# Performance work log

Measured on AMD Instinct MI355X. Metric: run time of the kernel, lower is better.

## Reference

```python
import jax, jax.numpy as jnp
import numpy as np
from jax import lax

EDGES = [(11,12),(11,23),(12,24),(23,24),(23,25),(25,27),(24,26),(26,28),(11,13),(13,15),(12,14),(14,16)]
J = 33

def _build_neighbors():
    nb = [[j] for j in range(J)]
    for a, b in EDGES:
        nb[a].append(b); nb[b].append(a)
    K = max(len(n) for n in nb)
    idx = np.zeros((J, K), np.int32)
    msk = np.zeros((J, K), np.float32)
    for j, n in enumerate(nb):
        idx[j, :len(n)] = n; msk[j, :len(n)] = 1.0
    return jnp.asarray(idx), jnp.asarray(msk)

NBR_IDX, NBR_MASK = _build_neighbors()
BN_EPS = 1e-5

def conv(x, w, b):
    y = lax.conv_general_dilated(x, w, (1, 1), 'SAME', dimension_numbers=('NCHW', 'OIHW', 'NCHW'))
    return y + b[None, :, None, None]

def bn(x, g, b):
    # eval-mode BatchNorm with running_mean=0, running_var=1
    s = g / jnp.sqrt(1.0 + BN_EPS)
    return x * s[None, :, None, None] + b[None, :, None, None]

def maxpool2(x):
    return lax.reduce_window(x, -jnp.inf, lax.max, (1, 1, 2, 2), (1, 1, 2, 2), 'VALID')

def deconv2x2(x, w, b):
    # ConvTranspose2d(k=2, s=2): w is [Cin, Cout, 2, 2]
    y = jnp.einsum('bcij,codk->boidjk', x, w)
    B, O, H, _, W, _ = y.shape
    return y.reshape(B, O, 2 * H, 2 * W) + b[None, :, None, None]

def forward(x, conv1_w, conv1_b, bn1_g, bn1_b, conv2_w, conv2_b, bn2_g, bn2_b,
            conv3_w, conv3_b, bn3_g, bn3_b, conv4_w, conv4_b, bn4_g, bn4_b,
            dc1_w, dc1_b, dc2_w, dc2_b, head_w, head_b, proj_w, proj_b,
            msg_w, msg_b, gru_w_ih, gru_w_hh, gru_b_ih, gru_b_hh,
            refine_w, refine_b, vis_w1, vis_b1, vis_w2, vis_b2):
    relu = jax.nn.relu
    h = bn(relu(conv(x, conv1_w, conv1_b)), bn1_g, bn1_b)
    h = bn(relu(conv(h, conv2_w, conv2_b)), bn2_g, bn2_b)
    h = maxpool2(h)
    h = bn(relu(conv(h, conv3_w, conv3_b)), bn3_g, bn3_b)
    h = maxpool2(h)
    enc = bn(relu(conv(h, conv4_w, conv4_b)), bn4_g, bn4_b)  # [B,256,H/4,W/4]
    f = relu(deconv2x2(enc, dc1_w, dc1_b))
    feat_map = relu(deconv2x2(f, dc2_w, dc2_b))  # [B,64,H,W]
    init_hm = jax.nn.sigmoid(conv(feat_map, head_w, head_b))  # [B,J,H,W]
    B, Jn, H, W = init_hm.shape
    sm = jax.nn.softmax(init_hm.reshape(B, Jn, H * W) / 0.1, axis=-1).reshape(B, Jn, H, W)
    w_idx = jnp.linspace(0.0, 1.0, W)
    h_idx = jnp.linspace(0.0, 1.0, H)
    pred_x = (sm.sum(-2) * w_idx).sum(-1)  # [B,J] in [0,1]
    pred_y = (sm.sum(-1) * h_idx).sum(-1)
    # grid_sample bilinear, align_corners=True: grid=(2p-1) -> pixel coord p*(dim-1)
    ix = pred_x * (W - 1)
    iy = pred_y * (H - 1)
    x0 = jnp.clip(jnp.floor(ix), 0, W - 1)
    y0 = jnp.clip(jnp.floor(iy), 0, H - 1)
    wx = ix - x0
    wy = iy - y0
    x0i = x0.astype(jnp.int32); x1i = jnp.clip(x0i + 1, 0, W - 1)
    y0i = y0.astype(jnp.int32); y1i = jnp.clip(y0i + 1, 0, H - 1)
    fm = feat_map.transpose(0, 2, 3, 1)  # [B,H,W,C]
    bidx = jnp.arange(B)[:, None]
    v00 = fm[bidx, y0i, x0i]; v01 = fm[bidx, y0i, x1i]
    v10 = fm[bidx, y1i, x0i]; v11 = fm[bidx, y1i, x1i]
    wx = wx[..., None]; wy = wy[..., None]
    joint = (v00 * (1 - wx) * (1 - wy) + v01 * wx * (1 - wy)
             + v10 * (1 - wx) * wy + v11 * wx * wy)  # [B,J,64]
    joint_feats = joint @ proj_w.T + proj_b
    # SkeletonGNN (all joints read original joint_feats -> fully parallel)
    gathered = joint_feats[:, NBR_IDX, :]  # [B,J,K,D]
    lin = gathered @ msg_w.T + msg_b
    m = NBR_MASK[None, :, :, None]
    msgs = (lin * m).sum(2) / NBR_MASK.sum(1)[None, :, None]  # [B,J,D]
    gi = msgs @ gru_w_ih.T + gru_b_ih
    gh = joint_feats @ gru_w_hh.T + gru_b_hh
    D = joint_feats.shape[-1]
    ir, iz, inn = gi[..., :D], gi[..., D:2 * D], gi[..., 2 * D:]
    hr, hz, hn = gh[..., :D], gh[..., D:2 * D], gh[..., 2 * D:]
    r = jax.nn.sigmoid(ir + hr)
    z = jax.nn.sigmoid(iz + hz)
    n = jnp.tanh(inn + r * hn)
    refined_feats = (1 - z) * n + z * joint_feats
    refined_bias = refined_feats.mean(-1)[:, :, None, None]
    refined_hm = jax.nn.sigmoid(conv(init_hm, refine_w, refine_b) + refined_bias)
    # visibility head: adaptive avg pool to 4x4 (enc HW divisible by 4), eval dropout = identity
    eB, eC, eH, eW = enc.shape
    p = enc.reshape(eB, eC, 4, eH // 4, 4, eW // 4).mean((3, 5))  # [B,256,4,4]
    v = jax.nn.relu(p.reshape(eB, -1) @ vis_w1.T + vis_b1)
    vis_pred = jax.nn.sigmoid(v @ vis_w2.T + vis_b2)
    return refined_hm, vis_pred

def setup_inputs() -> dict:
    key = jax.random.key(0)
    ks = iter(jax.random.split(key, 64))
    def w(shape, s=0.05):
        return (jax.random.normal(next(ks), shape, dtype=jnp.float32) * s)
    inp = {
        'x': jax.random.normal(next(ks), (16, 3, 256, 256), dtype=jnp.float32),
        'conv1_w': w((32, 3, 3, 3)), 'conv1_b': w((32,)), 'bn1_g': jnp.ones((32,)), 'bn1_b': jnp.zeros((32,)),
        'conv2_w': w((64, 32, 3, 3)), 'conv2_b': w((64,)), 'bn2_g': jnp.ones((64,)), 'bn2_b': jnp.zeros((64,)),
        'conv3_w': w((128, 64, 3, 3)), 'conv3_b': w((128,)), 'bn3_g': jnp.ones((128,)), 'bn3_b': jnp.zeros((128,)),
        'conv4_w': w((256, 128, 3, 3)), 'conv4_b': w((256,)), 'bn4_g': jnp.ones((256,)), 'bn4_b': jnp.zeros((256,)),
        'dc1_w': w((256, 128, 2, 2)), 'dc1_b': w((128,)),
        'dc2_w': w((128, 64, 2, 2)), 'dc2_b': w((64,)),
        'head_w': w((33, 64, 1, 1)), 'head_b': w((33,)),
        'proj_w': w((64, 64)), 'proj_b': w((64,)),
        'msg_w': w((64, 64)), 'msg_b': w((64,)),
        'gru_w_ih': w((192, 64)), 'gru_w_hh': w((192, 64)),
        'gru_b_ih': w((192,)), 'gru_b_hh': w((192,)),
        'refine_w': w((33, 33, 3, 3)), 'refine_b': w((33,)),
        'vis_w1': w((256, 256 * 16)), 'vis_b1': w((256,)),
        'vis_w2': w((33, 256)), 'vis_b2': w((33,)),
    }
    return inp

def reference(x, conv1_w, conv1_b, bn1_g, bn1_b, conv2_w, conv2_b, bn2_g, bn2_b,
              conv3_w, conv3_b, bn3_g, bn3_b, conv4_w, conv4_b, bn4_g, bn4_b,
              dc1_w, dc1_b, dc2_w, dc2_b, head_w, head_b, proj_w, proj_b,
              msg_w, msg_b, gru_w_ih, gru_w_hh, gru_b_ih, gru_b_hh,
              refine_w, refine_b, vis_w1, vis_b1, vis_w2, vis_b2):
    return forward(x, conv1_w, conv1_b, bn1_g, bn1_b, conv2_w, conv2_b, bn2_g, bn2_b,
                   conv3_w, conv3_b, bn3_g, bn3_b, conv4_w, conv4_b, bn4_g, bn4_b,
                   dc1_w, dc1_b, dc2_w, dc2_b, head_w, head_b, proj_w, proj_b,
                   msg_w, msg_b, gru_w_ih, gru_w_hh, gru_b_ih, gru_b_hh,
                   refine_w, refine_b, vis_w1, vis_b1, vis_w2, vis_b2)
```

## Files before the change

kernel.cpp:

```cpp
#include <hip/hip_runtime.h>
#include <hip/hip_bf16.h>
#include <math.h>

#define BN_RS 0.99999500003749977f

typedef __attribute__((ext_vector_type(8))) __bf16 bf16x8;
typedef __attribute__((ext_vector_type(4))) float f32x4;

union U16 { uint4 u; bf16x8 v; __hip_bfloat16 h[8]; };

__device__ __forceinline__ float sigf(float v) { return 1.0f / (1.0f + expf(-v)); }

__global__ __launch_bounds__(256)
void repack_conv_w_k(const float* __restrict__ w, __hip_bfloat16* __restrict__ wb,
                     int taps, int Co, int Ci, int CoT, int Kp)
{
    int i = blockIdx.x * 256 + threadIdx.x;
    int tot = taps * CoT * Kp;
    if (i >= tot) return;
    int k = i % Kp, n = (i / Kp) % CoT, t = i / (Kp * CoT);
    float v = (n < Co && k < Ci) ? w[((long)n * Ci + k) * taps + t] : 0.0f;
    wb[i] = __float2bfloat16(v);
}
__global__ __launch_bounds__(256)
void repack_deconv_w_k(const float* __restrict__ w, __hip_bfloat16* __restrict__ wb,
                       int Co, int Ci)
{
    int i = blockIdx.x * 256 + threadIdx.x;
    int tot = 4 * Co * Ci;
    if (i >= tot) return;
    int k = i % Ci, n = (i / Ci) % Co, q = i / (Ci * Co);
    wb[i] = __float2bfloat16(w[((long)k * Co + n) * 4 + q]);
}

__global__ __launch_bounds__(256)
void conv1_k(const float* __restrict__ x, const float* __restrict__ w,
             const float* __restrict__ cb, const float* __restrict__ g,
             const float* __restrict__ bb, __hip_bfloat16* __restrict__ out)
{
    __shared__ float sw[216];
    const int tid = threadIdx.x;
    const int b = blockIdx.z >> 2, cg = blockIdx.z & 3, co0 = cg * 8;
    for (int i = tid; i < 216; i += 256) {
        int t = i % 9, co = (i / 9) % 8, ci = i / 72;
        sw[i] = w[((co0 + co) * 3 + ci) * 9 + t];
    }
    __syncthreads();
    const int tx = tid & 15, ty = tid >> 4;
    const int y = blockIdx.y * 16 + ty;
    const int xs = blockIdx.x * 64 + tx;
    float acc[4][8];
#pragma unroll
    for (int p = 0; p < 4; ++p)
#pragma unroll
        for (int c = 0; c < 8; ++c) acc[p][c] = 0.0f;
    for (int ci = 0; ci < 3; ++ci) {
        const float* plane = x + ((long)b * 3 + ci) * 65536;
#pragma unroll
        for (int t = 0; t < 9; ++t) {
            const int dy = t / 3 - 1, dx = t % 3 - 1;
            const int yy = y + dy;
            if ((unsigned)yy < 256u) {
                const float* row = plane + yy * 256;
                float ws[8];
#pragma unroll
                for (int c = 0; c < 8; ++c) ws[c] = sw[ci * 72 + c * 9 + t];
#pragma unroll
                for (int p = 0; p < 4; ++p) {
                    const int xx = xs + p * 16 + dx;
                    const float v = ((unsigned)xx < 256u) ? row[xx] : 0.0f;
#pragma unroll
                    for (int c = 0; c < 8; ++c) acc[p][c] = fmaf(v, ws[c], acc[p][c]);
                }
            }
        }
    }
#pragma unroll
    for (int p = 0; p < 4; ++p) {
        U16 o;
#pragma unroll
        for (int c = 0; c < 8; ++c) {
            const int cc = co0 + c;
            float v = fmaxf(acc[p][c] + cb[cc], 0.0f) * (g[cc] * BN_RS) + bb[cc];
            o.h[c] = __float2bfloat16(v);
        }
        *(uint4*)(void*)(out + (((long)b * 65536 + (long)y * 256 + xs + p * 16) * 32 + co0)) = o.u;
    }
}

template<int MODE>
__global__ __launch_bounds__(256)
void mfma_conv_k(const __hip_bfloat16* __restrict__ in,
                 const __hip_bfloat16* __restrict__ wb,
                 const float* __restrict__ cbias,
                 const float* __restrict__ bng, const float* __restrict__ bnb,
                 const float* __restrict__ ebias,
                 __hip_bfloat16* __restrict__ out_bf, float* __restrict__ out_f32,
                 int H, int W, int Cin, int CoutT, int CG, int S)
{
    extern __shared__ float ltr[];
    const int tid = threadIdx.x;
    const int wid = tid >> 6, lane = tid & 63;
    const int ln = lane & 15, kg = lane >> 4;
    const int u = blockIdx.x * 4 + wid;
    const int y = u / S, x0 = (u % S) * 64;
    const int b = blockIdx.z / CG, cg = blockIdx.z % CG;
    const int co0 = cg * 64;
    const int KC = Cin >> 5;
    const long inb = (long)b * H * W * Cin;

    f32x4 acc[4][4];
#pragma unroll
    for (int i = 0; i < 4; ++i)
#pragma unroll
        for (int j = 0; j < 4; ++j) acc[i][j] = f32x4{0.f, 0.f, 0.f, 0.f};

    constexpr int NT = (MODE == 1) ? 1 : 9;
    for (int kc = 0; kc < KC; ++kc) {
        const int kofs = kc * 32 + kg * 8;
#pragma unroll
        for (int t = 0; t < NT; ++t) {
            const int dy = (MODE == 1) ? 0 : (t / 3 - 1);
            const int dx = (MODE == 1) ? 0 : (t % 3 - 1);
            bf16x8 bfr[4];
#pragma unroll
            for (int ni = 0; ni < 4; ++ni)
                bfr[ni] = *(const bf16x8*)(const void*)(wb + ((long)t * CoutT + co0 + ni * 16 + ln) * Cin + kofs);
            const int yy = y + dy;
            const bool rok = (unsigned)yy < (unsigned)H;
            const long rowb = inb + (long)yy * W * Cin;
#pragma unroll
            for (int mi = 0; mi < 4; ++mi) {
                const int xx = x0 + mi * 16 + ln + dx;
                U16 av;
                av.u = make_uint4(0u, 0u, 0u, 0u);
                if (rok && (unsigned)xx < (unsigned)W)
                    av.u = *(const uint4*)(const void*)(in + rowb + (long)xx * Cin + kofs);
#pragma unroll
                for (int ni = 0; ni < 4; ++ni)
                    acc[mi][ni] = __builtin_amdgcn_mfma_f32_16x16x32_bf16(av.v, bfr[ni], acc[mi][ni], 0, 0, 0);
            }
        }
    }

    if constexpr (MODE == 0) {
        const long ob = (long)b * H * W * CoutT;
#pragma unroll
        for (int mi = 0; mi < 4; ++mi) {
#pragma unroll
            for (int r = 0; r < 4; ++r) {
                const int px = x0 + mi * 16 + kg * 4 + r;
                const long pb = ob + ((long)y * W + px) * CoutT + co0;
#pragma unroll
                for (int ni = 0; ni < 4; ++ni) {
                    const int c = co0 + ni * 16 + ln;
                    float v = acc[mi][ni][r] + cbias[c];
                    v = fmaxf(v, 0.0f) * (bng[c] * BN_RS) + bnb[c];
                    out_bf[pb + ni * 16 + ln] = __float2bfloat16(v);
                }
            }
        }
    } else {
        float* wt = ltr + wid * 4160;
#pragma unroll
        for (int mi = 0; mi < 4; ++mi) {
#pragma unroll
            for (int r = 0; r < 4; ++r) {
                const int pxl = mi * 16 + kg * 4 + r;
                const int px = x0 + pxl;
#pragma unroll
                for (int ni = 0; ni < 4; ++ni) {
                    const int c = co0 + ni * 16 + ln;
                    float v = acc[mi][ni][r];
                    if constexpr (MODE == 1) {
                        v = sigf(v + ((c < 33) ? cbias[c] : 0.0f));
                        out_bf[(long)b * H * W * CoutT + ((long)y * W + px) * CoutT + c] =
                            (c < 33) ? __float2bfloat16(v) : __float2bfloat16(0.0f);
                    } else {
                        float eb = (c < 33) ? (cbias[c] + ebias[b * 33 + c]) : 0.0f;
                        v = sigf(v + eb);
                    }
                    wt[c * 65 + pxl] = v;
                }
            }
        }
        __syncthreads();
        const long o32 = ((long)b * 33) * H * W + (long)y * W + x0 + lane;
        for (int c = 0; c < 33; ++c)
            out_f32[o32 + (long)c * H * W] = wt[c * 65 + lane];
    }
}

__global__ __launch_bounds__(256)
void mfma_deconv_k(const __hip_bfloat16* __restrict__ in,
                   const __hip_bfloat16* __restrict__ wb,
                   const float* __restrict__ bias,
                   __hip_bfloat16* __restrict__ out,
                   int H, int W, int Cin, int CoutT, int CG, int S)
{
    const int tid = threadIdx.x;
    const int wid = tid >> 6, lane = tid & 63;
    const int ln = lane & 15, kg = lane >> 4;
    const int u = blockIdx.x * 4 + wid;
    const int y = u / S, x0 = (u % S) * 64;
    const int b = blockIdx.z / CG, cg = blockIdx.z % CG;
    const int co0 = cg * 64;
    const int KC = Cin >> 5;
    const long inb = (long)b * H * W * Cin;
    const int W2 = W * 2;
    const long ob = (long)b * 4 * H * W * CoutT;

    for (int q = 0; q < 4; ++q) {
        const int dy = q >> 1, dx = q & 1;
        f32x4 acc[4][4];
#pragma unroll
        for (int i = 0; i < 4; ++i)
#pragma unroll
            for (int j = 0; j < 4; ++j) acc[i][j] = f32x4{0.f, 0.f, 0.f, 0.f};
        for (int kc = 0; kc < KC; ++kc) {
            const int kofs = kc * 32 + kg * 8;
            bf16x8 bfr[4];
#pragma unroll
            for (int ni = 0; ni < 4; ++ni)
                bfr[ni] = *(const bf16x8*)(const void*)(wb + ((long)q * CoutT + co0 + ni * 16 + ln) * Cin + kofs);
#pragma unroll
            for (int mi = 0; mi < 4; ++mi) {
                const int xx = x0 + mi * 16 + ln;
                U16 av;
                av.u = *(const uint4*)(const void*)(in + inb + ((long)y * W + xx) * Cin + kofs);
#pragma unroll
                for (int ni = 0; ni < 4; ++ni)
                    acc[mi][ni] = __builtin_amdgcn_mfma_f32_16x16x32_bf16(av.v, bfr[ni], acc[mi][ni], 0, 0, 0);
            }
        }
#pragma unroll
        for (int mi = 0; mi < 4; ++mi) {
#pragma unroll
            for (int r = 0; r < 4; ++r) {
                const int xl = x0 + mi * 16 + kg * 4 + r;
                const long pb = ob + ((long)(2 * y + dy) * W2 + 2 * xl + dx) * CoutT + co0;
#pragma unroll
                for (int ni = 0; ni < 4; ++ni) {
                    const int c = co0 + ni * 16 + ln;
                    float v = fmaxf(acc[mi][ni][r] + bias[c], 0.0f);
                    out[pb + ni * 16 + ln] = __float2bfloat16(v);
                }
            }
        }
    }
}

__global__ __launch_bounds__(256)
void maxpool_bf_k(const __hip_bfloat16* __restrict__ in, __hip_bfloat16* __restrict__ out,
                  int Ho, int Wo, int C, long total)
{
    long idx = (long)blockIdx.x * 256 + threadIdx.x;
    if (idx >= total) return;
    const int ng = C >> 3;
    const int cg = (int)(idx % ng);
    long pix = idx / ng;
    const int xo = (int)(pix % Wo); pix /= Wo;
    const int yo = (int)(pix % Ho);
    const int b = (int)(pix / Ho);
    const int Wi = Wo * 2;
    const __hip_bfloat16* p = in + (((long)b * 2 * Ho + 2 * yo) * Wi + 2 * xo) * C + cg * 8;
    U16 a0, a1, a2, a3, o;
    a0.u = *(const uint4*)(const void*)p;
    a1.u = *(const uint4*)(const void*)(p + C);
    a2.u = *(const uint4*)(const void*)(p + (long)Wi * C);
    a3.u = *(const uint4*)(const void*)(p + (long)Wi * C + C);
#pragma unroll
    for (int j = 0; j < 8; ++j) {
        float m = fmaxf(fmaxf(__bfloat162float(a0.h[j]), __bfloat162float(a1.h[j])),
                        fmaxf(__bfloat162float(a2.h[j]), __bfloat162float(a3.h[j])));
        o.h[j] = __float2bfloat16(m);
    }
    *(uint4*)(void*)(out + (((long)b * Ho + yo) * Wo + xo) * C + cg * 8) = o.u;
}

__global__ __launch_bounds__(256)
void softargmax_k(const float* __restrict__ hm, float* __restrict__ coords)
{
    __shared__ float r0[256], r1[256], r2[256];
    const int bj = blockIdx.x;
    const int tid = threadIdx.x;
    const float* row = hm + (long)bj * 65536;
    float m = -1e30f;
    for (int i = tid; i < 65536; i += 256) m = fmaxf(m, row[i]);
    r0[tid] = m;
    __syncthreads();
    for (int s = 128; s > 0; s >>= 1) {
        if (tid < s) r0[tid] = fmaxf(r0[tid], r0[tid + s]);
        __syncthreads();
    }
    const float mx = r0[0];
    __syncthreads();
    float s = 0.0f, sx = 0.0f, sy = 0.0f;
    for (int i = tid; i < 65536; i += 256) {
        float e = expf((row[i] - mx) * 10.0f);
        s += e;
        sx += e * (float)(i & 255);
        sy += e * (float)(i >> 8);
    }
    r0[tid] = s; r1[tid] = sx; r2[tid] = sy;
    __syncthreads();
    for (int st = 128; st > 0; st >>= 1) {
        if (tid < st) { r0[tid] += r0[tid + st]; r1[tid] += r1[tid + st]; r2[tid] += r2[tid + st]; }
        __syncthreads();
    }
    if (tid == 0) {
        coords[2 * bj] = r1[0] / r0[0];
        coords[2 * bj + 1] = r2[0] / r0[0];
    }
}

__global__ __launch_bounds__(64)
void joint_bf_k(const __hip_bfloat16* __restrict__ fm, const float* __restrict__ coords,
                const float* __restrict__ pw, const float* __restrict__ pb,
                float* __restrict__ jf)
{
    __shared__ float sj[64];
    const int bj = blockIdx.x, b = bj / 33;
    const int tid = threadIdx.x;
    float ix = coords[2 * bj], iy = coords[2 * bj + 1];
    float x0f = fminf(fmaxf(floorf(ix), 0.0f), 255.0f);
    float y0f = fminf(fmaxf(floorf(iy), 0.0f), 255.0f);
    float wx = ix - x0f, wy = iy - y0f;
    int x0 = (int)x0f, y0 = (int)y0f;
    int x1 = min(x0 + 1, 255), y1 = min(y0 + 1, 255);
    const __hip_bfloat16* base = fm + (long)b * 65536 * 64 + tid;
    float v00 = __bfloat162float(base[((long)y0 * 256 + x0) * 64]);
    float v01 = __bfloat162float(base[((long)y0 * 256 + x1) * 64]);
    float v10 = __bfloat162float(base[((long)y1 * 256 + x0) * 64]);
    float v11 = __bfloat162float(base[((long)y1 * 256 + x1) * 64]);
    sj[tid] = v00 * (1 - wx) * (1 - wy) + v01 * wx * (1 - wy)
            + v10 * (1 - wx) * wy + v11 * wx * wy;
    __syncthreads();
    float a = pb[tid];
    for (int k = 0; k < 64; ++k) a = fmaf(sj[k], pw[tid * 64 + k], a);
    jf[(long)bj * 64 + tid] = a;
}

__device__ const int d_nbr[33][4] = {
    {0,0,0,0},{1,0,0,0},{2,0,0,0},{3,0,0,0},{4,0,0,0},{5,0,0,0},{6,0,0,0},{7,0,0,0},
    {8,0,0,0},{9,0,0,0},{10,0,0,0},
    {11,12,23,13},{12,11,24,14},{13,11,15,0},{14,12,16,0},{15,13,0,0},{16,14,0,0},
    {17,0,0,0},{18,0,0,0},{19,0,0,0},{20,0,0,0},{21,0,0,0},{22,0,0,0},
    {23,11,24,25},{24,12,23,26},{25,23,27,0},{26,24,28,0},{27,25,0,0},{28,26,0,0},
    {29,0,0,0},{30,0,0,0},{31,0,0,0},{32,0,0,0}};
__device__ const int d_cnt[33] = {1,1,1,1,1,1,1,1,1,1,1,4,4,3,3,2,2,1,1,1,1,1,1,4,4,3,3,2,2,1,1,1,1};

__global__ __launch_bounds__(192)
void gru_k(const float* __restrict__ jf, const float* __restrict__ mw, const float* __restrict__ mb,
           const float* __restrict__ wih, const float* __restrict__ whh,
           const float* __restrict__ bih, const float* __restrict__ bhh,
           float* __restrict__ rbias)
{
    __shared__ float s_mjf[64], s_jf[64], s_msg[64], s_gi[192], s_gh[192], s_ref[64];
    const int bj = blockIdx.x;
    const int b = bj / 33, j = bj % 33;
    const int tid = threadIdx.x;
    if (tid < 64) {
        int cnt = d_cnt[j];
        float s = 0.0f;
        for (int n = 0; n < 4; ++n)
            if (n < cnt) s += jf[((long)b * 33 + d_nbr[j][n]) * 64 + tid];
        s_mjf[tid] = s / (float)cnt;
        s_jf[tid] = jf[(long)bj * 64 + tid];
    }
    __syncthreads();
    if (tid < 64) {
        float a = mb[tid];
        for (int k = 0; k < 64; ++k) a = fmaf(mw[tid * 64 + k], s_mjf[k], a);
        s_msg[tid] = a;
    }
    __syncthreads();
    {
        float a = bih[tid], c = bhh[tid];
        for (int k = 0; k < 64; ++k) {
            a = fmaf(wih[tid * 64 + k], s_msg[k], a);
            c = fmaf(whh[tid * 64 + k], s_jf[k], c);
        }
        s_gi[tid] = a; s_gh[tid] = c;
    }
    __syncthreads();
    if (tid < 64) {
        float r = sigf(s_gi[tid] + s_gh[tid]);
        float z = sigf(s_gi[64 + tid] + s_gh[64 + tid]);
        float n = tanhf(s_gi[128 + tid] + r * s_gh[128 + tid]);
        s_ref[tid] = (1.0f - z) * n + z * s_jf[tid];
    }
    __syncthreads();
    if (tid == 0) {
        float s = 0.0f;
        for (int k = 0; k < 64; ++k) s += s_ref[k];
        rbias[bj] = s * (1.0f / 64.0f);
    }
}

__global__ __launch_bounds__(256)
void vispool_bf_k(const __hip_bfloat16* __restrict__ enc, float* __restrict__ p)
{
    int idx = blockIdx.x * 256 + threadIdx.x;
    int v = idx & 3, uu = (idx >> 2) & 3, c = (idx >> 4) & 255, b = idx >> 12;
    const __hip_bfloat16* base = enc + (long)b * 64 * 64 * 256 + c;
    float s = 0.0f;
    for (int a = 0; a < 16; ++a)
#pragma unroll
        for (int d = 0; d < 16; ++d)
            s += __bfloat162float(base[((long)(uu * 16 + a) * 64 + (v * 16 + d)) * 256]);
    p[idx] = s * (1.0f / 256.0f);
}

__global__ __launch_bounds__(256)
void visfc1_k(const float* __restrict__ p, const float* __restrict__ w1,
              const float* __restrict__ b1, float* __restrict__ v1)
{
    __shared__ float s_p[4096];
    const int b = blockIdx.x, tid = threadIdx.x;
    for (int i = tid; i < 4096; i += 256) s_p[i] = p[b * 4096 + i];
    __syncthreads();
    float a = b1[tid];
    const float* wr = w1 + (long)tid * 4096;
    for (int k = 0; k < 4096; ++k) a = fmaf(wr[k], s_p[k], a);
    v1[b * 256 + tid] = fmaxf(a, 0.0f);
}

__global__ __launch_bounds__(64)
void visfc2_k(const float* __restrict__ v1, const float* __restrict__ w2,
              const float* __restrict__ b2, float* __restrict__ out)
{
    const int b = blockIdx.x, t = threadIdx.x;
    if (t < 33) {
        float a = b2[t];
        for (int k = 0; k < 256; ++k) a = fmaf(w2[t * 256 + k], v1[b * 256 + k], a);
        out[b * 33 + t] = sigf(a);
    }
}

extern "C" void kernel_launch(void* const* d_in, const int* in_sizes, int n_in,
                              void* d_out, int out_size, void* d_ws, size_t ws_size,
                              hipStream_t stream)
{
    const float* x   = (const float*)d_in[0];
    const float* c1w = (const float*)d_in[1];  const float* c1b = (const float*)d_in[2];
    const float* b1g = (const float*)d_in[3];  const float* b1b = (const float*)d_in[4];
    const float* c2w = (const float*)d_in[5];  const float* c2b = (const float*)d_in[6];
    const float* b2g = (const float*)d_in[7];  const float* b2b = (const float*)d_in[8];
    const float* c3w = (const float*)d_in[9];  const float* c3b = (const float*)d_in[10];
    const float* b3g = (const float*)d_in[11]; const float* b3b = (const float*)d_in[12];
    const float* c4w = (const float*)d_in[13]; const float* c4b = (const float*)d_in[14];
    const float* b4g = (const float*)d_in[15]; const float* b4b = (const float*)d_in[16];
    const float* d1w = (const float*)d_in[17]; const float* d1b = (const float*)d_in[18];
    const float* d2w = (const float*)d_in[19]; const float* d2b = (const float*)d_in[20];
    const float* hw  = (const float*)d_in[21]; const float* hb  = (const float*)d_in[22];
    const float* pw  = (const float*)d_in[23]; const float* pb  = (const float*)d_in[24];
    const float* mw  = (const float*)d_in[25]; const float* mb  = (const float*)d_in[26];
    const float* wih = (const float*)d_in[27]; const float* whh = (const float*)d_in[28];
    const float* bih = (const float*)d_in[29]; const float* bhh = (const float*)d_in[30];
    const float* rw  = (const float*)d_in[31]; const float* rb  = (const float*)d_in[32];
    const float* v1w = (const float*)d_in[33]; const float* v1b = (const float*)d_in[34];
    const float* v2w = (const float*)d_in[35]; const float* v2b = (const float*)d_in[36];

    char* ws = (char*)d_ws;
    __hip_bfloat16* ENC    = (__hip_bfloat16*)(ws + 0L);
    __hip_bfloat16* FEAT   = (__hip_bfloat16*)(ws + 33554432L);
    __hip_bfloat16* HEADB  = (__hip_bfloat16*)(ws + 167772160L);
    float*          INITHM = (float*)(ws + 301989888L);
    __hip_bfloat16* H1     = (__hip_bfloat16*)(ws + 301989888L);
    __hip_bfloat16* H2     = (__hip_bfloat16*)(ws + 33554432L);
    __hip_bfloat16* P1     = (__hip_bfloat16*)(ws + 167772160L);
    __hip_bfloat16* H3     = (__hip_bfloat16*)(ws + 201326592L);
    __hip_bfloat16* P2     = (__hip_bfloat16*)(ws + 268435456L);
    __hip_bfloat16* F      = (__hip_bfloat16*)(ws + 167772160L);
    char* SM = ws + 440401920L;
    __hip_bfloat16* W2B = (__hip_bfloat16*)(SM + 0);
    __hip_bfloat16* W3B = (__hip_bfloat16*)(SM + 40960);
    __hip_bfloat16* W4B = (__hip_bfloat16*)(SM + 190464);
    __hip_bfloat16* WRB = (__hip_bfloat16*)(SM + 782336);
    __hip_bfloat16* WHB = (__hip_bfloat16*)(SM + 856064);
    __hip_bfloat16* WD1 = (__hip_bfloat16*)(SM + 866304);
    __hip_bfloat16* WD2 = (__hip_bfloat16*)(SM + 1128448);
    float* CO = (float*)(SM + 1196032);
    float* JF = (float*)(SM + 1200384);
    float* RB = (float*)(SM + 1335552);
    float* P  = (float*)(SM + 1337856);
    float* V1 = (float*)(SM + 1600000);

    float* out_hm  = (float*)d_out;
    float* out_vis = out_hm + 34603008L;

    repack_conv_w_k<<<(9*64*32 + 255)/256, 256, 0, stream>>>(c2w, W2B, 9, 64, 32, 64, 32);
    repack_conv_w_k<<<(9*128*64 + 255)/256, 256, 0, stream>>>(c3w, W3B, 9, 128, 64, 128, 64);
    repack_conv_w_k<<<(9*256*128 + 255)/256, 256, 0, stream>>>(c4w, W4B, 9, 256, 128, 256, 128);
    repack_conv_w_k<<<(9*64*64 + 255)/256, 256, 0, stream>>>(rw, WRB, 9, 33, 33, 64, 64);
    repack_conv_w_k<<<(1*64*64 + 255)/256, 256, 0, stream>>>(hw, WHB, 1, 33, 64, 64, 64);
    repack_deconv_w_k<<<(4*128*256 + 255)/256, 256, 0, stream>>>(d1w, WD1, 128, 256);
    repack_deconv_w_k<<<(4*64*128 + 255)/256, 256, 0, stream>>>(d2w, WD2, 64, 128);

    conv1_k<<<dim3(4, 16, 64), 256, 0, stream>>>(x, c1w, c1b, b1g, b1b, H1);
    mfma_conv_k<0><<<dim3(256, 1, 16), 256, 0, stream>>>(
        H1, W2B, c2b, b2g, b2b, nullptr, H2, nullptr, 256, 256, 32, 64, 1, 4);
    maxpool_bf_k<<<8192, 256, 0, stream>>>(H2, P1, 128, 128, 64, 2097152L);
    mfma_conv_k<0><<<dim3(64, 1, 32), 256, 0, stream>>>(
        P1, W3B, c3b, b3g, b3b, nullptr, H3, nullptr, 128, 128, 64, 128, 2, 2);
    maxpool_bf_k<<<4096, 256, 0, stream>>>(H3, P2, 64, 64, 128, 1048576L);
    mfma_conv_k<0><<<dim3(16, 1, 64), 256, 0, stream>>>(
        P2, W4B, c4b, b4g, b4b, nullptr, ENC, nullptr, 64, 64, 128, 256, 4, 1);
    mfma_deconv_k<<<dim3(16, 1, 32), 256, 0, stream>>>(
        ENC, WD1, d1b, F, 64, 64, 256, 128, 2, 1);
    mfma_deconv_k<<<dim3(64, 1, 16), 256, 0, stream>>>(
        F, WD2, d2b, FEAT, 128, 128, 128, 64, 1, 2);
    mfma_conv_k<1><<<dim3(256, 1, 16), 256, 66560, stream>>>(
        FEAT, WHB, hb, nullptr, nullptr, nullptr, HEADB, INITHM, 256, 256, 64, 64, 1, 4);
    softargmax_k<<<528, 256, 0, stream>>>(INITHM, CO);
    joint_bf_k<<<528, 64, 0, stream>>>(FEAT, CO, pw, pb, JF);
    gru_k<<<528, 192, 0, stream>>>(JF, mw, mb, wih, whh, bih, bhh, RB);
    mfma_conv_k<2><<<dim3(256, 1, 16), 256, 66560, stream>>>(
        HEADB, WRB, rb, nullptr, nullptr, RB, nullptr, out_hm, 256, 256, 64, 64, 1, 4);
    vispool_bf_k<<<256, 256, 0, stream>>>(ENC, P);
    visfc1_k<<<16, 256, 0, stream>>>(P, v1w, v1b, V1);
    visfc2_k<<<16, 64, 0, stream>>>(V1, v2w, v2b, out_vis);
}
```

Measured before the change: 1.821 ms.

## Use zero-padded halo buffers for 3x3 convs and trim head/refine MFMA tiles

Intermediate activations feeding the 3x3 convs are now stored in buffers with a one-pixel zero halo, written by a new zero_halo_k kernel. This lets the MFMA conv drop its per-load boundary checks and issue all four A loads before the MFMA loop. The head and refine convs use NI=3 output tiles instead of 4, which skips the padded channels beyond 48, and they use a smaller LDS transpose buffer. The __syncthreads before the per-wave transpose readback is removed. Buffers are reassigned, with H2 temporarily placed in the output buffer. This adds extra halo-zeroing launches and padded strides. The per-wave LDS readback has no barrier, which depends on lanes in a single wave staying in lockstep.

```diff
diff --git a/kernel.cpp b/kernel.cpp
--- a/kernel.cpp
+++ b/kernel.cpp
@@ -34,6 +34,30 @@
 }
 
 __global__ __launch_bounds__(256)
+void zero_halo_k(__hip_bfloat16* __restrict__ buf, int H, int W, int C, int B)
+{
+    const int P = W + 2;
+    const long per = (long)(2 * P + 2 * H) * C;
+    long idx = (long)blockIdx.x * 256 + threadIdx.x;
+    if (idx >= per * B) return;
+    int b = (int)(idx / per);
+    long r = idx % per;
+    long off;
+    if (r < (long)2 * P * C) {
+        int row = (r >= (long)P * C) ? (H + 1) : 0;
+        long r2 = r % ((long)P * C);
+        off = (((long)b * (H + 2) + row) * P) * C + r2;
+    } else {
+        long r2 = r - (long)2 * P * C;
+        int row = 1 + (int)(r2 / (2 * C));
+        int side = (int)((r2 / C) & 1);
+        int ch = (int)(r2 % C);
+        off = (((long)b * (H + 2) + row) * P + (side ? (W + 1) : 0)) * C + ch;
+    }
+    buf[off] = __float2bfloat16(0.0f);
+}
+
+__global__ __launch_bounds__(256)
 void conv1_k(const float* __restrict__ x, const float* __restrict__ w,
              const float* __restrict__ cb, const float* __restrict__ g,
              const float* __restrict__ bb, __hip_bfloat16* __restrict__ out)
@@ -62,15 +86,15 @@
             const int yy = y + dy;
             if ((unsigned)yy < 256u) {
                 const float* row = plane + yy * 256;
-                float ws[8];
-#pragma unroll
-                for (int c = 0; c < 8; ++c) ws[c] = sw[ci * 72 + c * 9 + t];
+                float wsr[8];
+#pragma unroll
+                for (int c = 0; c < 8; ++c) wsr[c] = sw[ci * 72 + c * 9 + t];
 #pragma unroll
                 for (int p = 0; p < 4; ++p) {
                     const int xx = xs + p * 16 + dx;
                     const float v = ((unsigned)xx < 256u) ? row[xx] : 0.0f;
 #pragma unroll
-                    for (int c = 0; c < 8; ++c) acc[p][c] = fmaf(v, ws[c], acc[p][c]);
+                    for (int c = 0; c < 8; ++c) acc[p][c] = fmaf(v, wsr[c], acc[p][c]);
                 }
             }
         }
@@ -84,11 +108,11 @@
             float v = fmaxf(acc[p][c] + cb[cc], 0.0f) * (g[cc] * BN_RS) + bb[cc];
             o.h[c] = __float2bfloat16(v);
         }
-        *(uint4*)(void*)(out + (((long)b * 65536 + (long)y * 256 + xs + p * 16) * 32 + co0)) = o.u;
-    }
-}
-
-template<int MODE>
+        *(uint4*)(void*)(out + ((long)b * 2130048L + ((long)y * 258 + xs + p * 16) * 32) + co0) = o.u;
+    }
+}
+
+template<int MODE, int NI>
 __global__ __launch_bounds__(256)
 void mfma_conv_k(const __hip_bfloat16* __restrict__ in,
                  const __hip_bfloat16* __restrict__ wb,
@@ -96,7 +120,8 @@
                  const float* __restrict__ bng, const float* __restrict__ bnb,
                  const float* __restrict__ ebias,
                  __hip_bfloat16* __restrict__ out_bf, float* __restrict__ out_f32,
-                 int H, int W, int Cin, int CoutT, int CG, int S)
+                 int H, int W, int Cin, int PIT, long bstride, long obstride, int OPIT,
+                 int CoutT, int CG, int S)
 {
     extern __shared__ float ltr[];
     const int tid = threadIdx.x;
@@ -107,13 +132,12 @@
     const int b = blockIdx.z / CG, cg = blockIdx.z % CG;
     const int co0 = cg * 64;
     const int KC = Cin >> 5;
-    const long inb = (long)b * H * W * Cin;
-
-    f32x4 acc[4][4];
+
+    f32x4 acc[4][NI];
 #pragma unroll
     for (int i = 0; i < 4; ++i)
 #pragma unroll
-        for (int j = 0; j < 4; ++j) acc[i][j] = f32x4{0.f, 0.f, 0.f, 0.f};
+        for (int j = 0; j < NI; ++j) acc[i][j] = f32x4{0.f, 0.f, 0.f, 0.f};
 
     constexpr int NT = (MODE == 1) ? 1 : 9;
     for (int kc = 0; kc < KC; ++kc) {
@@ -122,37 +146,32 @@
         for (int t = 0; t < NT; ++t) {
             const int dy = (MODE == 1) ? 0 : (t / 3 - 1);
             const int dx = (MODE == 1) ? 0 : (t % 3 - 1);
-            bf16x8 bfr[4];
-#pragma unroll
-            for (int ni = 0; ni < 4; ++ni)
-                bfr[ni] = *(const bf16x8*)(const void*)(wb + ((long)t * CoutT + co0 + ni * 16 + ln) * Cin + kofs);
-            const int yy = y + dy;
-            const bool rok = (unsigned)yy < (unsigned)H;
-            const long rowb = inb + (long)yy * W * Cin;
-#pragma unroll
-            for (int mi = 0; mi < 4; ++mi) {
-                const int xx = x0 + mi * 16 + ln + dx;
-                U16 av;
-                av.u = make_uint4(0u, 0u, 0u, 0u);
-                if (rok && (unsigned)xx < (unsigned)W)
-                    av.u = *(const uint4*)(const void*)(in + rowb + (long)xx * Cin + kofs);
-#pragma unroll
-                for (int ni = 0; ni < 4; ++ni)
-                    acc[mi][ni] = __builtin_amdgcn_mfma_f32_16x16x32_bf16(av.v, bfr[ni], acc[mi][ni], 0, 0, 0);
-            }
+            bf16x8 wfr[NI];
+#pragma unroll
+            for (int ni = 0; ni < NI; ++ni)
+                wfr[ni] = *(const bf16x8*)(const void*)(wb + ((long)t * CoutT + co0 + ni * 16 + ln) * Cin + kofs);
+            U16 av[4];
+            const long rowb = (long)b * bstride + (long)(y + dy) * PIT * Cin + kofs;
+#pragma unroll
+            for (int mi = 0; mi < 4; ++mi)
+                av[mi].u = *(const uint4*)(const void*)(in + rowb + (long)(x0 + mi * 16 + ln + dx) * Cin);
+#pragma unroll
+            for (int mi = 0; mi < 4; ++mi)
+#pragma unroll
+                for (int ni = 0; ni < NI; ++ni)
+                    acc[mi][ni] = __builtin_amdgcn_mfma_f32_16x16x32_bf16(av[mi].v, wfr[ni], acc[mi][ni], 0, 0, 0);
         }
     }
 
     if constexpr (MODE == 0) {
-        const long ob = (long)b * H * W * CoutT;
 #pragma unroll
         for (int mi = 0; mi < 4; ++mi) {
 #pragma unroll
             for (int r = 0; r < 4; ++r) {
                 const int px = x0 + mi * 16 + kg * 4 + r;
-                const long pb = ob + ((long)y * W + px) * CoutT + co0;
-#pragma unroll
-                for (int ni = 0; ni < 4; ++ni) {
+                const long pb = (long)b * obstride + ((long)y * OPIT + px) * CoutT + co0;
+#pragma unroll
+                for (int ni = 0; ni < NI; ++ni) {
                     const int c = co0 + ni * 16 + ln;
                     float v = acc[mi][ni][r] + cbias[c];
                     v = fmaxf(v, 0.0f) * (bng[c] * BN_RS) + bnb[c];
@@ -161,33 +180,31 @@
             }
         }
     } else {
-        float* wt = ltr + wid * 4160;
+        float* wt = ltr + wid * (48 * 67);
 #pragma unroll
         for (int mi = 0; mi < 4; ++mi) {
 #pragma unroll
             for (int r = 0; r < 4; ++r) {
                 const int pxl = mi * 16 + kg * 4 + r;
-                const int px = x0 + pxl;
-#pragma unroll
-                for (int ni = 0; ni < 4; ++ni) {
-                    const int c = co0 + ni * 16 + ln;
+#pragma unroll
+                for (int ni = 0; ni < NI; ++ni) {
+                    const int c = ni * 16 + ln;
                     float v = acc[mi][ni][r];
                     if constexpr (MODE == 1) {
                         v = sigf(v + ((c < 33) ? cbias[c] : 0.0f));
-                        out_bf[(long)b * H * W * CoutT + ((long)y * W + px) * CoutT + c] =
+                        out_bf[(long)b * obstride + ((long)y * OPIT + x0 + pxl) * CoutT + c] =
                             (c < 33) ? __float2bfloat16(v) : __float2bfloat16(0.0f);
                     } else {
                         float eb = (c < 33) ? (cbias[c] + ebias[b * 33 + c]) : 0.0f;
                         v = sigf(v + eb);
                     }
-                    wt[c * 65 + pxl] = v;
+                    wt[c * 67 + pxl] = v;
                 }
             }
         }
-        __syncthreads();
         const long o32 = ((long)b * 33) * H * W + (long)y * W + x0 + lane;
         for (int c = 0; c < 33; ++c)
-            out_f32[o32 + (long)c * H * W] = wt[c * 65 + lane];
+            out_f32[o32 + (long)c * H * W] = wt[c * 67 + lane];
     }
 }
 
@@ -219,19 +236,19 @@
             for (int j = 0; j < 4; ++j) acc[i][j] = f32x4{0.f, 0.f, 0.f, 0.f};
         for (int kc = 0; kc < KC; ++kc) {
             const int kofs = kc * 32 + kg * 8;
-            bf16x8 bfr[4];
+            bf16x8 wfr[4];
+            U16 av[4];
 #pragma unroll
             for (int ni = 0; ni < 4; ++ni)
-                bfr[ni] = *(const bf16x8*)(const void*)(wb + ((long)q * CoutT + co0 + ni * 16 + ln) * Cin + kofs);
-#pragma unroll
-            for (int mi = 0; mi < 4; ++mi) {
-                const int xx = x0 + mi * 16 + ln;
-                U16 av;
-                av.u = *(const uint4*)(const void*)(in + inb + ((long)y * W + xx) * Cin + kofs);
+                wfr[ni] = *(const bf16x8*)(const void*)(wb + ((long)q * CoutT + co0 + ni * 16 + ln) * Cin + kofs);
+#pragma unroll
+            for (int mi = 0; mi < 4; ++mi)
+                av[mi].u = *(const uint4*)(const void*)(in + inb + ((long)y * W + x0 + mi * 16 + ln) * Cin + kofs);
+#pragma unroll
+            for (int mi = 0; mi < 4; ++mi)
 #pragma unroll
                 for (int ni = 0; ni < 4; ++ni)
-                    acc[mi][ni] = __builtin_amdgcn_mfma_f32_16x16x32_bf16(av.v, bfr[ni], acc[mi][ni], 0, 0, 0);
-            }
+                    acc[mi][ni] = __builtin_amdgcn_mfma_f32_16x16x32_bf16(av[mi].v, wfr[ni], acc[mi][ni], 0, 0, 0);
         }
 #pragma unroll
         for (int mi = 0; mi < 4; ++mi) {
@@ -252,7 +269,7 @@
 
 __global__ __launch_bounds__(256)
 void maxpool_bf_k(const __hip_bfloat16* __restrict__ in, __hip_bfloat16* __restrict__ out,
-                  int Ho, int Wo, int C, long total)
+                  int Ho, int Wo, int C, long total, int OPIT, long obstride)
 {
     long idx = (long)blockIdx.x * 256 + threadIdx.x;
     if (idx >= total) return;
@@ -275,7 +292,7 @@
                         fmaxf(__bfloat162float(a2.h[j]), __bfloat162float(a3.h[j])));
         o.h[j] = __float2bfloat16(m);
     }
-    *(uint4*)(void*)(out + (((long)b * Ho + yo) * Wo + xo) * C + cg * 8) = o.u;
+    *(uint4*)(void*)(out + (long)b * obstride + ((long)yo * OPIT + xo) * C + cg * 8) = o.u;
 }
 
 __global__ __launch_bounds__(256)
@@ -463,32 +480,37 @@
     const float* v2w = (const float*)d_in[35]; const float* v2b = (const float*)d_in[36];
 
     char* ws = (char*)d_ws;
-    __hip_bfloat16* ENC    = (__hip_bfloat16*)(ws + 0L);
-    __hip_bfloat16* FEAT   = (__hip_bfloat16*)(ws + 33554432L);
-    __hip_bfloat16* HEADB  = (__hip_bfloat16*)(ws + 167772160L);
-    float*          INITHM = (float*)(ws + 301989888L);
-    __hip_bfloat16* H1     = (__hip_bfloat16*)(ws + 301989888L);
-    __hip_bfloat16* H2     = (__hip_bfloat16*)(ws + 33554432L);
-    __hip_bfloat16* P1     = (__hip_bfloat16*)(ws + 167772160L);
-    __hip_bfloat16* H3     = (__hip_bfloat16*)(ws + 201326592L);
-    __hip_bfloat16* P2     = (__hip_bfloat16*)(ws + 268435456L);
-    __hip_bfloat16* F      = (__hip_bfloat16*)(ws + 167772160L);
-    char* SM = ws + 440401920L;
+    __hip_bfloat16* ENC  = (__hip_bfloat16*)(ws + 0L);
+    __hip_bfloat16* R1   = (__hip_bfloat16*)(ws + 33554432L);
+    __hip_bfloat16* R2   = (__hip_bfloat16*)(ws + 167772160L);
+    char*           R3c  = ws + 304095232L;
+    char* SM = ws + 442507264L;
+
+    __hip_bfloat16* H1B = R1;                 __hip_bfloat16* H1I = R1 + 8288;
+    __hip_bfloat16* P1B = R1;                 __hip_bfloat16* P1I = R1 + 8384;
+    __hip_bfloat16* FEAT = R1;
+    __hip_bfloat16* H3  = R2;
+    __hip_bfloat16* F   = R2;
+    __hip_bfloat16* HDB = R2;                 __hip_bfloat16* HDI = R2 + 16576;
+    __hip_bfloat16* P2B = (__hip_bfloat16*)R3c; __hip_bfloat16* P2I = P2B + 8576;
+    float*          INITHM = (float*)R3c;
+
     __hip_bfloat16* W2B = (__hip_bfloat16*)(SM + 0);
-    __hip_bfloat16* W3B = (__hip_bfloat16*)(SM + 40960);
-    __hip_bfloat16* W4B = (__hip_bfloat16*)(SM + 190464);
-    __hip_bfloat16* WRB = (__hip_bfloat16*)(SM + 782336);
-    __hip_bfloat16* WHB = (__hip_bfloat16*)(SM + 856064);
-    __hip_bfloat16* WD1 = (__hip_bfloat16*)(SM + 866304);
-    __hip_bfloat16* WD2 = (__hip_bfloat16*)(SM + 1128448);
-    float* CO = (float*)(SM + 1196032);
-    float* JF = (float*)(SM + 1200384);
-    float* RB = (float*)(SM + 1335552);
-    float* P  = (float*)(SM + 1337856);
-    float* V1 = (float*)(SM + 1600000);
+    __hip_bfloat16* W3B = (__hip_bfloat16*)(SM + 36864);
+    __hip_bfloat16* W4B = (__hip_bfloat16*)(SM + 184320);
+    __hip_bfloat16* WRB = (__hip_bfloat16*)(SM + 774144);
+    __hip_bfloat16* WHB = (__hip_bfloat16*)(SM + 847872);
+    __hip_bfloat16* WD1 = (__hip_bfloat16*)(SM + 856064);
+    __hip_bfloat16* WD2 = (__hip_bfloat16*)(SM + 1118208);
+    float* CO = (float*)(SM + 1183744);
+    float* JF = (float*)(SM + 1187968);
+    float* RB = (float*)(SM + 1323136);
+    float* P  = (float*)(SM + 1325248);
+    float* V1 = (float*)(SM + 1587392);
 
     float* out_hm  = (float*)d_out;
     float* out_vis = out_hm + 34603008L;
+    __hip_bfloat16* H2 = (__hip_bfloat16*)d_out;
 
     repack_conv_w_k<<<(9*64*32 + 255)/256, 256, 0, stream>>>(c2w, W2B, 9, 64, 32, 64, 32);
     repack_conv_w_k<<<(9*128*64 + 255)/256, 256, 0, stream>>>(c3w, W3B, 9, 128, 64, 128, 64);
@@ -498,26 +520,36 @@
     repack_deconv_w_k<<<(4*128*256 + 255)/256, 256, 0, stream>>>(d1w, WD1, 128, 256);
     repack_deconv_w_k<<<(4*64*128 + 255)/256, 256, 0, stream>>>(d2w, WD2, 64, 128);
 
-    conv1_k<<<dim3(4, 16, 64), 256, 0, stream>>>(x, c1w, c1b, b1g, b1b, H1);
-    mfma_conv_k<0><<<dim3(256, 1, 16), 256, 0, stream>>>(
-        H1, W2B, c2b, b2g, b2b, nullptr, H2, nullptr, 256, 256, 32, 64, 1, 4);
-    maxpool_bf_k<<<8192, 256, 0, stream>>>(H2, P1, 128, 128, 64, 2097152L);
-    mfma_conv_k<0><<<dim3(64, 1, 32), 256, 0, stream>>>(
-        P1, W3B, c3b, b3g, b3b, nullptr, H3, nullptr, 128, 128, 64, 128, 2, 2);
-    maxpool_bf_k<<<4096, 256, 0, stream>>>(H3, P2, 64, 64, 128, 1048576L);
-    mfma_conv_k<0><<<dim3(16, 1, 64), 256, 0, stream>>>(
-        P2, W4B, c4b, b4g, b4b, nullptr, ENC, nullptr, 64, 64, 128, 256, 4, 1);
+    zero_halo_k<<<(526336 + 255)/256, 256, 0, stream>>>(H1B, 256, 256, 32, 16);
+    zero_halo_k<<<(532480 + 255)/256, 256, 0, stream>>>(P2B, 64, 64, 128, 16);
+
+    conv1_k<<<dim3(4, 16, 64), 256, 0, stream>>>(x, c1w, c1b, b1g, b1b, H1I);
+    mfma_conv_k<0, 4><<<dim3(256, 1, 16), 256, 0, stream>>>(
+        H1I, W2B, c2b, b2g, b2b, nullptr, H2, nullptr,
+        256, 256, 32, 258, 2130048L, 4194304L, 256, 64, 1, 4);
+    zero_halo_k<<<(528384 + 255)/256, 256, 0, stream>>>(P1B, 128, 128, 64, 16);
+    maxpool_bf_k<<<8192, 256, 0, stream>>>(H2, P1I, 128, 128, 64, 2097152L, 130, 1081600L);
+    mfma_conv_k<0, 4><<<dim3(64, 1, 32), 256, 0, stream>>>(
+        P1I, W3B, c3b, b3g, b3b, nullptr, H3, nullptr,
+        128, 128, 64, 130, 1081600L, 2097152L, 128, 128, 2, 2);
+    maxpool_bf_k<<<4096, 256, 0, stream>>>(H3, P2I, 64, 64, 128, 1048576L, 66, 557568L);
+    mfma_conv_k<0, 4><<<dim3(16, 1, 64), 256, 0, stream>>>(
+        P2I, W4B, c4b, b4g, b4b, nullptr, ENC, nullptr,
+        64, 64, 128, 66, 557568L, 1048576L, 64, 256, 4, 1);
     mfma_deconv_k<<<dim3(16, 1, 32), 256, 0, stream>>>(
         ENC, WD1, d1b, F, 64, 64, 256, 128, 2, 1);
     mfma_deconv_k<<<dim3(64, 1, 16), 256, 0, stream>>>(
         F, WD2, d2b, FEAT, 128, 128, 128, 64, 1, 2);
-    mfma_conv_k<1><<<dim3(256, 1, 16), 256, 66560, stream>>>(
-        FEAT, WHB, hb, nullptr, nullptr, nullptr, HEADB, INITHM, 256, 256, 64, 64, 1, 4);
+    zero_halo_k<<<(1052672 + 255)/256, 256, 0, stream>>>(HDB, 256, 256, 64, 16);
+    mfma_conv_k<1, 3><<<dim3(256, 1, 16), 256, 51456, stream>>>(
+        FEAT, WHB, hb, nullptr, nullptr, nullptr, HDI, INITHM,
+        256, 256, 64, 256, 4194304L, 4260096L, 258, 64, 1, 4);
     softargmax_k<<<528, 256, 0, stream>>>(INITHM, CO);
     joint_bf_k<<<528, 64, 0, stream>>>(FEAT, CO, pw, pb, JF);
     gru_k<<<528, 192, 0, stream>>>(JF, mw, mb, wih, whh, bih, bhh, RB);
-    mfma_conv_k<2><<<dim3(256, 1, 16), 256, 66560, stream>>>(
-        HEADB, WRB, rb, nullptr, nullptr, RB, nullptr, out_hm, 256, 256, 64, 64, 1, 4);
+    mfma_conv_k<2, 3><<<dim3(256, 1, 16), 256, 51456, stream>>>(
+        HDI, WRB, rb, nullptr, nullptr, RB, nullptr, out_hm,
+        256, 256, 64, 258, 4260096L, 0L, 0, 64, 1, 4);
     vispool_bf_k<<<256, 256, 0, stream>>>(ENC, P);
     visfc1_k<<<16, 256, 0, stream>>>(P, v1w, v1b, V1);
     visfc2_k<<<16, 64, 0, stream>>>(V1, v2w, v2b, out_vis);
```

Measured after the change: 1.562 ms. 1.17x faster.
